# Optimization experiments

Measured on AMD Instinct MI355X. Metric: run time of the kernel, lower is better.

Reference implementation:

```python
import jax, jax.numpy as jnp
import numpy as np

EPS = 1e-10


def _gcn(X, A, W, act):
    # A_hat = A + I; symmetric normalization D^{-1/2} A_hat D^{-1/2}
    N = A.shape[0]
    A_hat = A + jnp.eye(N, dtype=A.dtype)
    d = 1.0 / jnp.sqrt(jnp.sum(A_hat, axis=1) + EPS)
    A_norm = (d[:, None] * A_hat) * d[None, :]  # same math as diag @ A_hat @ diag
    return act(A_norm @ (X @ W))


def _pool(X, A, s, k):
    scores = (X @ s)[:, 0]            # [N]
    _, idx = jax.lax.top_k(scores, k)  # static k (ceil(ratio*N))
    return X[idx], A[idx][:, idx], idx


def _unpool(Xp, idx, N):
    return jnp.zeros((N, Xp.shape[-1]), Xp.dtype).at[idx].set(Xp)


def _glorot(key, shape):
    lim = np.sqrt(6.0 / (shape[0] + shape[1])).astype(np.float32)
    return jax.random.uniform(key, shape, jnp.float32, -lim, lim)


def setup_inputs() -> dict:
    key = jax.random.key(0)
    ks = jax.random.split(key, 8)
    N, F_IN, F, C = 8192, 16, 32, 2
    x = jax.random.normal(ks[0], (N, F_IN), jnp.float32)
    # sparse-ish symmetric binary adjacency stored densely (as the module expects)
    a = (jax.random.uniform(ks[1], (N, N)) < 0.01).astype(jnp.float32)
    a = jnp.maximum(a, a.T)
    return {
        "x": x,
        "a": a,
        "W1": _glorot(ks[2], (F_IN, F)),
        "W2": _glorot(ks[3], (F, F)),
        "W3": _glorot(ks[4], (F, F)),
        "W4": _glorot(ks[5], (F, C)),
        "s1": _glorot(ks[6], (F, 1)),
        "s2": _glorot(ks[7], (F, 1)),
    }


def reference(x, a, W1, W2, W3, W4, s1, s2):
    N = x.shape[0]
    K1 = int(np.ceil(0.5 * N))   # pool1 ratio 0.5
    K2 = int(np.ceil(0.5 * K1))  # pool2 ratio 0.5
    relu = jax.nn.relu
    X1 = _gcn(x, a, W1, relu)                     # [N, F]
    X1p, A1p, idx1 = _pool(X1, a, s1, K1)         # [K1, F], [K1, K1]
    X2 = _gcn(X1p, A1p, W2, relu)                 # [K1, F]
    X2p, _, idx2 = _pool(X2, A1p, s2, K2)         # [K2, F]
    X3 = _unpool(X2p, idx2, K1)                   # scatter back to [K1, F]
    X3 = _gcn(X3, A1p, W3, relu)
    X4 = _unpool(X3, idx1, N)                     # scatter back to [N, F]
    return _gcn(X4, a, W4, lambda z: jax.nn.softmax(z, axis=-1))
```

## Files before the change

### kernel.cpp

```cpp
#include <hip/hip_runtime.h>
#include <stdint.h>

#define NNODES 8192
#define KP1 4096
#define KP2 2048
#define FIN 16
#define FH 32
#define COUT 2
#define STRA 320
#define STRS 320
#define CGRID 1024
#define GRPSH 5
#define GRPSZ 32
#define BARWORDS (66 * 32)
#define RNONE 0xFFFFu

typedef unsigned short u16;
typedef unsigned int u32;
typedef unsigned long long u64;

__device__ __forceinline__ void st_u32(void* p, u32 v)
{
    __hip_atomic_store((u32*)p, v, __ATOMIC_RELAXED, __HIP_MEMORY_SCOPE_AGENT);
}
__device__ __forceinline__ void st_f32(float* p, float v) { st_u32(p, __float_as_uint(v)); }
__device__ __forceinline__ void st_u64(void* p, u64 v)
{
    __hip_atomic_store((u64*)p, v, __ATOMIC_RELAXED, __HIP_MEMORY_SCOPE_AGENT);
}

__global__ __launch_bounds__(256) void build_ell(const float* __restrict__ A, int n, int stride,
        u16* __restrict__ ell, int* __restrict__ rowcnt, int* __restrict__ diag, float* __restrict__ dnorm,
        const float* __restrict__ Xf, const float* __restrict__ Wf, float* __restrict__ Zf, int kf,
        u32* __restrict__ bar)
{
    if ((int)blockIdx.x >= n) {
        if ((int)blockIdx.x == n) {
            for (int w = threadIdx.x; w < BARWORDS; w += 256)
                __hip_atomic_store(&bar[w], 0u, __ATOMIC_RELAXED, __HIP_MEMORY_SCOPE_AGENT);
        }
        int t = ((int)blockIdx.x - n) * 256 + threadIdx.x;
        int i = t >> 5;
        int f = t & 31;
        const float* xr = Xf + (size_t)i * kf;
        float acc = 0.0f;
        for (int k = 0; k < kf; ++k) acc += xr[k] * Wf[k * 32 + f];
        Zf[t] = acc;
        return;
    }
    __shared__ int cnt;
    __shared__ int dg;
    int row = blockIdx.x;
    if (threadIdx.x == 0) { cnt = 0; dg = 0; }
    __syncthreads();
    const float4* arow4 = (const float4*)(A + (size_t)row * n);
    u16* erow = ell + (size_t)row * stride;
    int n4 = n >> 2;
    for (int c4 = threadIdx.x; c4 < n4; c4 += 256) {
        float4 v = arow4[c4];
        if (v.x == 0.0f && v.y == 0.0f && v.z == 0.0f && v.w == 0.0f) continue;
        int cb = c4 << 2;
        if (v.x != 0.0f) {
            if (cb == row) dg = 1;
            else { int p = atomicAdd(&cnt, 1); if (p < stride) erow[p] = (u16)cb; }
        }
        if (v.y != 0.0f) {
            int c = cb + 1;
            if (c == row) dg = 1;
            else { int p = atomicAdd(&cnt, 1); if (p < stride) erow[p] = (u16)c; }
        }
        if (v.z != 0.0f) {
            int c = cb + 2;
            if (c == row) dg = 1;
            else { int p = atomicAdd(&cnt, 1); if (p < stride) erow[p] = (u16)c; }
        }
        if (v.w != 0.0f) {
            int c = cb + 3;
            if (c == row) dg = 1;
            else { int p = atomicAdd(&cnt, 1); if (p < stride) erow[p] = (u16)c; }
        }
    }
    __syncthreads();
    if (threadIdx.x == 0) {
        int cf = cnt;
        rowcnt[row] = cf < stride ? cf : stride;
        diag[row] = dg;
        dnorm[row] = rsqrtf((float)(cf + dg + 1) + 1e-10f);
    }
}

__device__ __forceinline__ void gbar(u32* bar, int bid, int nblk)
{
    __syncthreads();
    if (threadIdx.x == 0) {
        asm volatile("s_waitcnt vmcnt(0)" ::: "memory");
        int g = bid >> GRPSH;
        int ngrp = (nblk + GRPSZ - 1) >> GRPSH;
        int gsz = nblk - (g << GRPSH); if (gsz > GRPSZ) gsz = GRPSZ;
        u32* gcnt = bar + (size_t)g * 32;
        u32* ggen = bar + (size_t)(32 + g) * 32;
        u32* rcnt = bar + (size_t)64 * 32;
        u32* rgen = bar + (size_t)65 * 32;
        u32 sg = __hip_atomic_load(ggen, __ATOMIC_RELAXED, __HIP_MEMORY_SCOPE_AGENT);
        u32 a = __hip_atomic_fetch_add(gcnt, 1u, __ATOMIC_RELAXED, __HIP_MEMORY_SCOPE_AGENT);
        if (a == (u32)(gsz - 1)) {
            u32 sr = __hip_atomic_load(rgen, __ATOMIC_RELAXED, __HIP_MEMORY_SCOPE_AGENT);
            u32 r = __hip_atomic_fetch_add(rcnt, 1u, __ATOMIC_RELAXED, __HIP_MEMORY_SCOPE_AGENT);
            if (r == (u32)(ngrp - 1)) {
                __hip_atomic_store(rcnt, 0u, __ATOMIC_RELAXED, __HIP_MEMORY_SCOPE_AGENT);
                __hip_atomic_fetch_add(rgen, 1u, __ATOMIC_RELAXED, __HIP_MEMORY_SCOPE_AGENT);
            } else {
                while (__hip_atomic_load(rgen, __ATOMIC_RELAXED, __HIP_MEMORY_SCOPE_AGENT) == sr)
                    __builtin_amdgcn_s_sleep(2);
            }
            __hip_atomic_store(gcnt, 0u, __ATOMIC_RELAXED, __HIP_MEMORY_SCOPE_AGENT);
            __hip_atomic_fetch_add(ggen, 1u, __ATOMIC_RELAXED, __HIP_MEMORY_SCOPE_AGENT);
        } else {
            while (__hip_atomic_load(ggen, __ATOMIC_RELAXED, __HIP_MEMORY_SCOPE_AGENT) == sg)
                __builtin_amdgcn_s_sleep(4);
        }
    }
    __syncthreads();
}

struct TkS {
    u32 hist[4][256];
    u32 wsum[4];
    u32 pref;
    u32 rem;
};

__device__ __forceinline__ u32 km_of(float f)
{
    u32 u = __float_as_uint(f);
    u32 m;
    if (u & 0x80000000u) m = ~u; else m = u | 0x80000000u;
    return ~m;
}

__device__ void topk_local(TkS& s, u16* rank_l, u16* idx_l,
                           const float* __restrict__ scores, int n, int K, int tid,
                           int* __restrict__ grank, int* __restrict__ gidx, bool mirror)
{
    int wv = tid >> 6;
    int lane = tid & 63;
    int per = n >> 8;
    int base = tid * per;
    if (tid == 0) { s.pref = 0u; s.rem = (u32)K; }
    __syncthreads();
    for (int bp = 3; bp >= 0; --bp) {
        s.hist[0][tid] = 0u;
        s.hist[1][tid] = 0u;
        s.hist[2][tid] = 0u;
        s.hist[3][tid] = 0u;
        __syncthreads();
        u32 maskhi = 0u;
        if (bp < 3) maskhi = 0xFFFFFFFFu << ((bp + 1) * 8);
        u32 pref = s.pref;
        u32 rem = s.rem;
        for (int e = 0; e < per; ++e) {
            u32 km = km_of(scores[base + e]);
            if ((km & maskhi) == pref) atomicAdd(&s.hist[wv][(km >> (bp * 8)) & 255u], 1u);
        }
        __syncthreads();
        u32 tot = s.hist[0][tid] + s.hist[1][tid] + s.hist[2][tid] + s.hist[3][tid];
        u32 vv = tot;
        u32 t2;
        t2 = __shfl(vv, lane - 1);  if (lane >= 1)  vv += t2;
        t2 = __shfl(vv, lane - 2);  if (lane >= 2)  vv += t2;
        t2 = __shfl(vv, lane - 4);  if (lane >= 4)  vv += t2;
        t2 = __shfl(vv, lane - 8);  if (lane >= 8)  vv += t2;
        t2 = __shfl(vv, lane - 16); if (lane >= 16) vv += t2;
        t2 = __shfl(vv, lane - 32); if (lane >= 32) vv += t2;
        if (lane == 63) s.wsum[wv] = vv;
        __syncthreads();
        u32 add = 0u;
        if (wv > 0) add += s.wsum[0];
        if (wv > 1) add += s.wsum[1];
        if (wv > 2) add += s.wsum[2];
        u32 cum = vv + add;
        if (tot != 0u && cum >= rem && cum - tot < rem) {
            s.pref = pref | ((u32)tid << (bp * 8));
            s.rem = rem - (cum - tot);
        }
    }
    __syncthreads();
    u32 T = s.pref;
    u32 need_eq = s.rem;
    u32 run = 0u;
    for (int e = 0; e < per; ++e) {
        u32 km = km_of(scores[base + e]);
        if (km < T) run += 0x10000u;
        else if (km == T) run += 1u;
    }
    u32 v2 = run;
    u32 t3;
    t3 = __shfl(v2, lane - 1);  if (lane >= 1)  v2 += t3;
    t3 = __shfl(v2, lane - 2);  if (lane >= 2)  v2 += t3;
    t3 = __shfl(v2, lane - 4);  if (lane >= 4)  v2 += t3;
    t3 = __shfl(v2, lane - 8);  if (lane >= 8)  v2 += t3;
    t3 = __shfl(v2, lane - 16); if (lane >= 16) v2 += t3;
    t3 = __shfl(v2, lane - 32); if (lane >= 32) v2 += t3;
    if (lane == 63) s.wsum[wv] = v2;
    __syncthreads();
    u32 add2 = 0u;
    if (wv > 0) add2 += s.wsum[0];
    if (wv > 1) add2 += s.wsum[1];
    if (wv > 2) add2 += s.wsum[2];
    u32 cur = v2 + add2 - run;
    for (int e = 0; e < per; ++e) {
        int v = base + e;
        u32 km = km_of(scores[v]);
        u32 ltb = cur >> 16;
        u32 eqb = cur & 0xFFFFu;
        u32 eqs = eqb < need_eq ? eqb : need_eq;
        int sel = 0;
        if (km < T) { sel = 1; cur += 0x10000u; }
        else if (km == T) { if (eqb < need_eq) sel = 1; cur += 1u; }
        if (sel) {
            int r = (int)(ltb + eqs);
            rank_l[v] = (u16)r;
            idx_l[r] = (u16)v;
            if (mirror) { st_u32(&grank[v], (u32)r); st_u32(&gidx[r], (u32)v); }
        } else {
            rank_l[v] = RNONE;
            if (mirror) st_u32(&grank[v], 0xFFFFFFFFu);
        }
    }
    __syncthreads();
}

template<typename ET, bool REMAP, bool MASK, bool FW4, bool SC, bool EPI>
__device__ __forceinline__ void spmm_phase(
        const ET* __restrict__ ell, const int* __restrict__ rowcnt,
        const int* __restrict__ diag, const float* __restrict__ dnorm,
        const float* __restrict__ Z, const int* __restrict__ remap, const u16* mask_l,
        float* __restrict__ scores, const float* __restrict__ svec,
        const float* __restrict__ Wn, float* __restrict__ Zn,
        int n, int stride, int gwave, int nwaves, int lane)
{
    int g = lane >> 3;
    int q = lane & 7;
    for (int wid = gwave; wid < n; wid += nwaves) {
        int cnt = rowcnt[wid];
        const ET* erow = ell + (size_t)wid * stride;
        float ax = 0.0f, ay = 0.0f, az = 0.0f, aw = 0.0f;
        for (int it = g; it < cnt; it += 8) {
            int c = (int)erow[it];
            if (MASK && mask_l[c] == RNONE) continue;
            int zc = REMAP ? remap[c] : c;
            float dn = dnorm[c];
            const float4* zp = (const float4*)(Z + (size_t)zc * 32);
            float4 zv = zp[q];
            ax += dn * zv.x;
            ay += dn * zv.y;
            az += dn * zv.z;
            aw += dn * zv.w;
        }
        ax += __shfl_xor(ax, 8);  ay += __shfl_xor(ay, 8);
        az += __shfl_xor(az, 8);  aw += __shfl_xor(aw, 8);
        ax += __shfl_xor(ax, 16); ay += __shfl_xor(ay, 16);
        az += __shfl_xor(az, 16); aw += __shfl_xor(aw, 16);
        ax += __shfl_xor(ax, 32); ay += __shfl_xor(ay, 32);
        az += __shfl_xor(az, 32); aw += __shfl_xor(aw, 32);
        float ox = 0.0f, oy = 0.0f, oz = 0.0f, ow = 0.0f;
        if (g == 0) {
            float dr = dnorm[wid];
            bool selfok = !(MASK && mask_l[wid] == RNONE);
            if (selfok) {
                int zc = REMAP ? remap[wid] : wid;
                const float4* zp = (const float4*)(Z + (size_t)zc * 32);
                float4 zv = zp[q];
                float cf = (float)(diag[wid] + 1) * dr;
                ax += cf * zv.x;
                ay += cf * zv.y;
                az += cf * zv.z;
                aw += cf * zv.w;
            }
            ox = fmaxf(dr * ax, 0.0f);
            oy = fmaxf(dr * ay, 0.0f);
            oz = fmaxf(dr * az, 0.0f);
            ow = fmaxf(dr * aw, 0.0f);
            if (FW4) {
                int kb = q * 4;
                float p0 = ox * Wn[(kb + 0) * 2 + 0] + oy * Wn[(kb + 1) * 2 + 0]
                         + oz * Wn[(kb + 2) * 2 + 0] + ow * Wn[(kb + 3) * 2 + 0];
                float p1 = ox * Wn[(kb + 0) * 2 + 1] + oy * Wn[(kb + 1) * 2 + 1]
                         + oz * Wn[(kb + 2) * 2 + 1] + ow * Wn[(kb + 3) * 2 + 1];
                p0 += __shfl_xor(p0, 1);
                p1 += __shfl_xor(p1, 1);
                p0 += __shfl_xor(p0, 2);
                p1 += __shfl_xor(p1, 2);
                p0 += __shfl_xor(p0, 4);
                p1 += __shfl_xor(p1, 4);
                if (q == 0) {
                    union { float2 f; u64 u; } cv;
                    cv.f.x = p0;
                    cv.f.y = p1;
                    st_u64(&((float2*)Zn)[wid], cv.u);
                }
            } else if (SC) {
                const float4* sp = (const float4*)svec;
                float4 sv = sp[q];
                float pp = ox * sv.x + oy * sv.y + oz * sv.z + ow * sv.w;
                pp += __shfl_xor(pp, 1);
                pp += __shfl_xor(pp, 2);
                pp += __shfl_xor(pp, 4);
                if (q == 0) st_f32(&scores[wid], pp);
            }
        }
        if (EPI) {
            int f = lane & 31;
            float acc = 0.0f;
#pragma unroll
            for (int k = 0; k < 32; ++k) {
                float comp = ((k & 3) == 0) ? ox : ((k & 3) == 1) ? oy
                           : ((k & 3) == 2) ? oz : ow;
                float rowk = __shfl(comp, k >> 2);
                acc += rowk * Wn[k * 32 + f];
            }
            if (lane < 32) st_f32(&Zn[(size_t)wid * 32 + f], acc);
        }
    }
}

__device__ __forceinline__ void subell_phase(const u16* __restrict__ ellA, const int* __restrict__ rowcntA,
        const int* __restrict__ diagA, const u16* idx_l, const u16* rank_l,
        u32* __restrict__ ellS, int* __restrict__ rowcntS, int* __restrict__ diagS, float* __restrict__ dnormS,
        int k1, int strideA, int strideS, int gwave, int nwaves, int lane)
{
    for (int wid = gwave; wid < k1; wid += nwaves) {
        int r = idx_l[wid];
        int cnt = rowcntA[r];
        const u16* erow = ellA + (size_t)r * strideA;
        u32* srow = ellS + (size_t)wid * strideS;
        int outn = 0;
        for (int t0 = 0; t0 < cnt; t0 += 64) {
            int it = t0 + lane;
            u16 rk = RNONE;
            if (it < cnt) rk = rank_l[erow[it]];
            unsigned long long b = __ballot(rk != RNONE);
            int ofs = __popcll(b & ((1ull << lane) - 1ull));
            if (rk != RNONE) st_u32(&srow[outn + ofs], (u32)rk);
            outn += __popcll(b);
        }
        if (lane == 0) {
            int dg = diagA[r];
            st_u32(&rowcntS[wid], (u32)outn);
            st_u32(&diagS[wid], (u32)dg);
            st_f32(&dnormS[wid], rsqrtf((float)(outn + dg + 1) + 1e-10f));
        }
    }
}

__device__ __forceinline__ void spmmout_phase(const u16* __restrict__ ell, const int* __restrict__ rowcnt,
        const int* __restrict__ diag, const float* __restrict__ dnorm, const float* __restrict__ Zr,
        const int* __restrict__ gat, float* __restrict__ out, int n, int stride,
        int gwave, int nwaves, int lane)
{
    const float2* Z2 = (const float2*)Zr;
    for (int wid = gwave; wid < n; wid += nwaves) {
        int cnt = rowcnt[wid];
        const u16* erow = ell + (size_t)wid * stride;
        float ax = 0.0f, ay = 0.0f;
        for (int it = lane; it < cnt; it += 64) {
            int c = erow[it];
            int rk = gat[c];
            if (rk >= 0) {
                float dn = dnorm[c];
                float2 zv = Z2[rk];
                ax += dn * zv.x;
                ay += dn * zv.y;
            }
        }
        ax += __shfl_xor(ax, 1);  ay += __shfl_xor(ay, 1);
        ax += __shfl_xor(ax, 2);  ay += __shfl_xor(ay, 2);
        ax += __shfl_xor(ax, 4);  ay += __shfl_xor(ay, 4);
        ax += __shfl_xor(ax, 8);  ay += __shfl_xor(ay, 8);
        ax += __shfl_xor(ax, 16); ay += __shfl_xor(ay, 16);
        ax += __shfl_xor(ax, 32); ay += __shfl_xor(ay, 32);
        if (lane == 0) {
            float dr = dnorm[wid];
            int rks = gat[wid];
            if (rks >= 0) {
                float cf = (float)(diag[wid] + 1) * dr;
                float2 zs = Z2[rks];
                ax += cf * zs.x;
                ay += cf * zs.y;
            }
            float v0 = dr * ax;
            float v1 = dr * ay;
            float m = fmaxf(v0, v1);
            float e0 = __expf(v0 - m);
            float e1 = __expf(v1 - m);
            float inv = 1.0f / (e0 + e1);
            float2 r;
            r.x = e0 * inv;
            r.y = e1 * inv;
            ((float2*)out)[wid] = r;
        }
    }
}

struct GcnP {
    const u16* ellA; const int* cntA; const int* diagA; const float* dnA;
    const float* Z1; float* sc1; int* rank1; int* idx1;
    u32* ellS; int* cntS; int* diagS; float* dnS;
    float* Z2f; float* sc2;
    float* Z3f; float* Z4r;
    const float* W2; const float* W3; const float* W4; const float* s1; const float* s2;
    float* out;
    u32* bar;
};

__global__ __launch_bounds__(256, 4) void gcn_pipeline(GcnP p)
{
    __shared__ TkS sm;
    __shared__ u16 rank_l[NNODES];
    __shared__ u16 idx_l[KP1];
    int tid = threadIdx.x;
    int bid = blockIdx.x;
    int lane = tid & 63;
    int gwave = (bid * 256 + tid) >> 6;
    int nwaves = ((int)gridDim.x * 256) >> 6;
    int nblk = (int)gridDim.x;

    spmm_phase<u16, false, false, false, true, true>(p.ellA, p.cntA, p.diagA, p.dnA, p.Z1,
        (const int*)0, (const u16*)0, p.sc1, p.s1, p.W2, p.Z2f,
        NNODES, STRA, gwave, nwaves, lane);
    gbar(p.bar, bid, nblk);

    topk_local(sm, rank_l, idx_l, p.sc1, NNODES, KP1, tid, p.rank1, p.idx1, bid == 0);
    subell_phase(p.ellA, p.cntA, p.diagA, idx_l, rank_l, p.ellS, p.cntS, p.diagS, p.dnS,
        KP1, STRA, STRS, gwave, nwaves, lane);
    gbar(p.bar, bid, nblk);

    spmm_phase<u32, true, false, false, true, true>(p.ellS, p.cntS, p.diagS, p.dnS, p.Z2f,
        p.idx1, (const u16*)0, p.sc2, p.s2, p.W3, p.Z3f,
        KP1, STRS, gwave, nwaves, lane);
    gbar(p.bar, bid, nblk);

    topk_local(sm, rank_l, idx_l, p.sc2, KP1, KP2, tid, (int*)0, (int*)0, false);
    spmm_phase<u32, false, true, true, false, false>(p.ellS, p.cntS, p.diagS, p.dnS, p.Z3f,
        (const int*)0, rank_l, (float*)0, (const float*)0, p.W4, p.Z4r,
        KP1, STRS, gwave, nwaves, lane);
    gbar(p.bar, bid, nblk);

    spmmout_phase(p.ellA, p.cntA, p.diagA, p.dnA, p.Z4r, p.rank1, p.out,
        NNODES, STRA, gwave, nwaves, lane);
}

__global__ __launch_bounds__(256) void k_spmmA(const u16* __restrict__ ell, const int* __restrict__ rowcnt,
        const int* __restrict__ diag, const float* __restrict__ dnorm, const float* __restrict__ Z,
        float* __restrict__ scores, const float* __restrict__ svec,
        const float* __restrict__ Wn, float* __restrict__ Zn, int n, int stride)
{
    int gwave = ((int)blockIdx.x * 256 + (int)threadIdx.x) >> 6;
    int nwaves = ((int)gridDim.x * 256) >> 6;
    spmm_phase<u16, false, false, false, true, true>(ell, rowcnt, diag, dnorm, Z,
        (const int*)0, (const u16*)0, scores, svec, Wn, Zn, n, stride, gwave, nwaves, threadIdx.x & 63);
}

__global__ __launch_bounds__(256) void k_phaseB(const float* __restrict__ scores,
        int* __restrict__ grank, int* __restrict__ gidx,
        const u16* __restrict__ ellA, const int* __restrict__ rowcntA, const int* __restrict__ diagA,
        u32* __restrict__ ellS, int* __restrict__ rowcntS, int* __restrict__ diagS, float* __restrict__ dnormS)
{
    __shared__ TkS sm;
    __shared__ u16 rank_l[NNODES];
    __shared__ u16 idx_l[KP1];
    int gwave = ((int)blockIdx.x * 256 + (int)threadIdx.x) >> 6;
    int nwaves = ((int)gridDim.x * 256) >> 6;
    topk_local(sm, rank_l, idx_l, scores, NNODES, KP1, threadIdx.x, grank, gidx, blockIdx.x == 0);
    subell_phase(ellA, rowcntA, diagA, idx_l, rank_l, ellS, rowcntS, diagS, dnormS,
        KP1, STRA, STRS, gwave, nwaves, threadIdx.x & 63);
}

__global__ __launch_bounds__(256) void k_spmmC(const u32* __restrict__ ell, const int* __restrict__ rowcnt,
        const int* __restrict__ diag, const float* __restrict__ dnorm, const float* __restrict__ Z,
        const int* __restrict__ remap, float* __restrict__ scores, const float* __restrict__ svec,
        const float* __restrict__ Wn, float* __restrict__ Zn, int n, int stride)
{
    int gwave = ((int)blockIdx.x * 256 + (int)threadIdx.x) >> 6;
    int nwaves = ((int)gridDim.x * 256) >> 6;
    spmm_phase<u32, true, false, false, true, true>(ell, rowcnt, diag, dnorm, Z,
        remap, (const u16*)0, scores, svec, Wn, Zn, n, stride, gwave, nwaves, threadIdx.x & 63);
}

__global__ __launch_bounds__(256) void k_phaseD(const float* __restrict__ scores,
        const u32* __restrict__ ell, const int* __restrict__ rowcnt,
        const int* __restrict__ diag, const float* __restrict__ dnorm, const float* __restrict__ Z,
        const float* __restrict__ Wn, float* __restrict__ Zn, int n, int stride)
{
    __shared__ TkS sm;
    __shared__ u16 rank_l[NNODES];
    __shared__ u16 idx_l[KP1];
    int gwave = ((int)blockIdx.x * 256 + (int)threadIdx.x) >> 6;
    int nwaves = ((int)gridDim.x * 256) >> 6;
    topk_local(sm, rank_l, idx_l, scores, KP1, KP2, threadIdx.x, (int*)0, (int*)0, false);
    spmm_phase<u32, false, true, true, false, false>(ell, rowcnt, diag, dnorm, Z,
        (const int*)0, rank_l, (float*)0, (const float*)0, Wn, Zn, n, stride, gwave, nwaves, threadIdx.x & 63);
}

__global__ __launch_bounds__(256) void k_spmmout(const u16* __restrict__ ell, const int* __restrict__ rowcnt,
        const int* __restrict__ diag, const float* __restrict__ dnorm, const float* __restrict__ Zr,
        const int* __restrict__ gat, float* __restrict__ out, int n, int stride)
{
    int gwave = ((int)blockIdx.x * 256 + (int)threadIdx.x) >> 6;
    int nwaves = ((int)gridDim.x * 256) >> 6;
    spmmout_phase(ell, rowcnt, diag, dnorm, Zr, gat, out, n, stride, gwave, nwaves, threadIdx.x & 63);
}

#define CARVE(type, name, bytes) \
    type name = (type)wp; wp += (((size_t)(bytes)) + 255) & ~((size_t)255);

extern "C" void kernel_launch(void* const* d_in, const int* in_sizes, int n_in,
                              void* d_out, int out_size, void* d_ws, size_t ws_size,
                              hipStream_t stream)
{
    const float* x  = (const float*)d_in[0];
    const float* a  = (const float*)d_in[1];
    const float* W1 = (const float*)d_in[2];
    const float* W2 = (const float*)d_in[3];
    const float* W3 = (const float*)d_in[4];
    const float* W4 = (const float*)d_in[5];
    const float* s1 = (const float*)d_in[6];
    const float* s2 = (const float*)d_in[7];
    float* out = (float*)d_out;
    (void)in_sizes; (void)n_in; (void)out_size; (void)ws_size;

    char* wp = (char*)d_ws;
    CARVE(u16*,   ellA,  (size_t)NNODES * STRA * sizeof(u16));
    CARVE(int*,   cntA,  NNODES * sizeof(int));
    CARVE(int*,   diagA, NNODES * sizeof(int));
    CARVE(float*, dnA,   NNODES * sizeof(float));
    CARVE(float*, Z1,    (size_t)NNODES * FH * sizeof(float));
    CARVE(float*, sc1,   NNODES * sizeof(float));
    CARVE(int*,   rank1, NNODES * sizeof(int));
    CARVE(int*,   idx1,  NNODES * sizeof(int));
    CARVE(u32*,   ellS,  (size_t)KP1 * STRS * sizeof(u32));
    CARVE(int*,   cntS,  KP1 * sizeof(int));
    CARVE(int*,   diagS, KP1 * sizeof(int));
    CARVE(float*, dnS,   KP1 * sizeof(float));
    CARVE(float*, Z2f,   (size_t)NNODES * FH * sizeof(float));
    CARVE(float*, sc2,   KP1 * sizeof(float));
    CARVE(float*, Z3f,   (size_t)KP1 * FH * sizeof(float));
    CARVE(float*, Z4r,   (size_t)KP1 * COUT * sizeof(float));
    CARVE(u32*,   barws, BARWORDS * sizeof(u32));

    build_ell<<<NNODES + (NNODES * FH) / 256, 256, 0, stream>>>(
        a, NNODES, STRA, ellA, cntA, diagA, dnA, x, W1, Z1, FIN, barws);

    static int g_ok = -1;
    if (g_ok < 0) {
        int maxb = 0;
        int ncu = 0;
        hipDeviceProp_t props;
        if (hipOccupancyMaxActiveBlocksPerMultiprocessor(&maxb, (const void*)gcn_pipeline, 256, 0)
                == hipSuccess
            && hipGetDeviceProperties(&props, 0) == hipSuccess)
            ncu = props.multiProcessorCount;
        g_ok = ((long)maxb * (long)ncu >= CGRID) ? 1 : 0;
    }

    if (g_ok) {
        GcnP pp;
        pp.ellA = ellA; pp.cntA = cntA; pp.diagA = diagA; pp.dnA = dnA;
        pp.Z1 = Z1; pp.sc1 = sc1; pp.rank1 = rank1; pp.idx1 = idx1;
        pp.ellS = ellS; pp.cntS = cntS; pp.diagS = diagS; pp.dnS = dnS;
        pp.Z2f = Z2f; pp.sc2 = sc2;
        pp.Z3f = Z3f; pp.Z4r = Z4r;
        pp.W2 = W2; pp.W3 = W3; pp.W4 = W4; pp.s1 = s1; pp.s2 = s2;
        pp.out = out;
        pp.bar = barws;
        gcn_pipeline<<<CGRID, 256, 0, stream>>>(pp);
    } else {
        k_spmmA<<<NNODES / 4, 256, 0, stream>>>(ellA, cntA, diagA, dnA, Z1,
            sc1, s1, W2, Z2f, NNODES, STRA);
        k_phaseB<<<KP1 / 4, 256, 0, stream>>>(sc1, rank1, idx1,
            ellA, cntA, diagA, ellS, cntS, diagS, dnS);
        k_spmmC<<<KP1 / 4, 256, 0, stream>>>(ellS, cntS, diagS, dnS, Z2f,
            idx1, sc2, s2, W3, Z3f, KP1, STRS);
        k_phaseD<<<KP1 / 4, 256, 0, stream>>>(sc2, ellS, cntS, diagS, dnS, Z3f,
            W4, Z4r, KP1, STRS);
        k_spmmout<<<NNODES / 4, 256, 0, stream>>>(ellA, cntA, diagA, dnA, Z4r, rank1, out, NNODES, STRA);
    }
}
```

Measured before the change: 524.6 us.

## Fuse ELL construction into persistent pipeline and aggregate topk histogram atomics

Moves the dense-to-ELL adjacency conversion and the X@W1 product into the persistent cooperative kernel. Each block now processes 8 rows, staging column indices in shared memory and writing them out as packed u32 pairs, and a grid barrier separates this stage from the first SpMM. The barrier words are cleared with hipMemsetAsync instead of by the removed launch. Separately, the top-k radix histogram now uses wave-level ballot aggregation so each distinct bin gets one atomic per wave. The intent is to remove a kernel launch and reduce shared-atomic contention, but only 1024 blocks now stream the 256MB adjacency matrix instead of 8192, which may lower memory parallelism.

```diff
diff --git a/kernel.cpp b/kernel.cpp
--- a/kernel.cpp
+++ b/kernel.cpp
@@ -10,6 +10,7 @@
 #define STRA 320
 #define STRS 320
 #define CGRID 1024
+#define ROWS_PB (NNODES / CGRID)
 #define GRPSH 5
 #define GRPSZ 32
 #define BARWORDS (66 * 32)
@@ -27,66 +28,6 @@
 __device__ __forceinline__ void st_u64(void* p, u64 v)
 {
     __hip_atomic_store((u64*)p, v, __ATOMIC_RELAXED, __HIP_MEMORY_SCOPE_AGENT);
-}
-
-__global__ __launch_bounds__(256) void build_ell(const float* __restrict__ A, int n, int stride,
-        u16* __restrict__ ell, int* __restrict__ rowcnt, int* __restrict__ diag, float* __restrict__ dnorm,
-        const float* __restrict__ Xf, const float* __restrict__ Wf, float* __restrict__ Zf, int kf,
-        u32* __restrict__ bar)
-{
-    if ((int)blockIdx.x >= n) {
-        if ((int)blockIdx.x == n) {
-            for (int w = threadIdx.x; w < BARWORDS; w += 256)
-                __hip_atomic_store(&bar[w], 0u, __ATOMIC_RELAXED, __HIP_MEMORY_SCOPE_AGENT);
-        }
-        int t = ((int)blockIdx.x - n) * 256 + threadIdx.x;
-        int i = t >> 5;
-        int f = t & 31;
-        const float* xr = Xf + (size_t)i * kf;
-        float acc = 0.0f;
-        for (int k = 0; k < kf; ++k) acc += xr[k] * Wf[k * 32 + f];
-        Zf[t] = acc;
-        return;
-    }
-    __shared__ int cnt;
-    __shared__ int dg;
-    int row = blockIdx.x;
-    if (threadIdx.x == 0) { cnt = 0; dg = 0; }
-    __syncthreads();
-    const float4* arow4 = (const float4*)(A + (size_t)row * n);
-    u16* erow = ell + (size_t)row * stride;
-    int n4 = n >> 2;
-    for (int c4 = threadIdx.x; c4 < n4; c4 += 256) {
-        float4 v = arow4[c4];
-        if (v.x == 0.0f && v.y == 0.0f && v.z == 0.0f && v.w == 0.0f) continue;
-        int cb = c4 << 2;
-        if (v.x != 0.0f) {
-            if (cb == row) dg = 1;
-            else { int p = atomicAdd(&cnt, 1); if (p < stride) erow[p] = (u16)cb; }
-        }
-        if (v.y != 0.0f) {
-            int c = cb + 1;
-            if (c == row) dg = 1;
-            else { int p = atomicAdd(&cnt, 1); if (p < stride) erow[p] = (u16)c; }
-        }
-        if (v.z != 0.0f) {
-            int c = cb + 2;
-            if (c == row) dg = 1;
-            else { int p = atomicAdd(&cnt, 1); if (p < stride) erow[p] = (u16)c; }
-        }
-        if (v.w != 0.0f) {
-            int c = cb + 3;
-            if (c == row) dg = 1;
-            else { int p = atomicAdd(&cnt, 1); if (p < stride) erow[p] = (u16)c; }
-        }
-    }
-    __syncthreads();
-    if (threadIdx.x == 0) {
-        int cf = cnt;
-        rowcnt[row] = cf < stride ? cf : stride;
-        diag[row] = dg;
-        dnorm[row] = rsqrtf((float)(cf + dg + 1) + 1e-10f);
-    }
 }
 
 __device__ __forceinline__ void gbar(u32* bar, int bid, int nblk)
@@ -160,7 +101,16 @@
         u32 rem = s.rem;
         for (int e = 0; e < per; ++e) {
             u32 km = km_of(scores[base + e]);
-            if ((km & maskhi) == pref) atomicAdd(&s.hist[wv][(km >> (bp * 8)) & 255u], 1u);
+            bool prd = ((km & maskhi) == pref);
+            u32 bin = (km >> (bp * 8)) & 255u;
+            u64 todo = __ballot(prd);
+            while (todo) {
+                int ldr = __ffsll((long long)todo) - 1;
+                u32 lbin = __shfl(bin, ldr);
+                u64 same = __ballot(prd && (bin == lbin));
+                if (lane == ldr) atomicAdd(&s.hist[wv][lbin], (u32)__popcll(same));
+                todo &= ~same;
+            }
         }
         __syncthreads();
         u32 tot = s.hist[0][tid] + s.hist[1][tid] + s.hist[2][tid] + s.hist[3][tid];
@@ -403,8 +353,9 @@
 }
 
 struct GcnP {
-    const u16* ellA; const int* cntA; const int* diagA; const float* dnA;
-    const float* Z1; float* sc1; int* rank1; int* idx1;
+    const float* A; const float* x; const float* W1;
+    u16* ellA; int* cntA; int* diagA; float* dnA;
+    float* Z1; float* sc1; int* rank1; int* idx1;
     u32* ellS; int* cntS; int* diagS; float* dnS;
     float* Z2f; float* sc2;
     float* Z3f; float* Z4r;
@@ -418,6 +369,8 @@
     __shared__ TkS sm;
     __shared__ u16 rank_l[NNODES];
     __shared__ u16 idx_l[KP1];
+    __shared__ u16 colbuf[STRA];
+    __shared__ int scnt, sdg;
     int tid = threadIdx.x;
     int bid = blockIdx.x;
     int lane = tid & 63;
@@ -425,6 +378,65 @@
     int nwaves = ((int)gridDim.x * 256) >> 6;
     int nblk = (int)gridDim.x;
 
+    for (int rr = 0; rr < ROWS_PB; ++rr) {
+        int row = bid * ROWS_PB + rr;
+        if (tid == 0) { scnt = 0; sdg = 0; }
+        __syncthreads();
+        const float4* arow4 = (const float4*)(p.A + (size_t)row * NNODES);
+        int n4 = NNODES >> 2;
+        for (int c4 = tid; c4 < n4; c4 += 256) {
+            float4 v = arow4[c4];
+            if (v.x == 0.0f && v.y == 0.0f && v.z == 0.0f && v.w == 0.0f) continue;
+            int cb = c4 << 2;
+            if (v.x != 0.0f) {
+                if (cb == row) sdg = 1;
+                else { int pp = atomicAdd(&scnt, 1); if (pp < STRA) colbuf[pp] = (u16)cb; }
+            }
+            if (v.y != 0.0f) {
+                int c = cb + 1;
+                if (c == row) sdg = 1;
+                else { int pp = atomicAdd(&scnt, 1); if (pp < STRA) colbuf[pp] = (u16)c; }
+            }
+            if (v.z != 0.0f) {
+                int c = cb + 2;
+                if (c == row) sdg = 1;
+                else { int pp = atomicAdd(&scnt, 1); if (pp < STRA) colbuf[pp] = (u16)c; }
+            }
+            if (v.w != 0.0f) {
+                int c = cb + 3;
+                if (c == row) sdg = 1;
+                else { int pp = atomicAdd(&scnt, 1); if (pp < STRA) colbuf[pp] = (u16)c; }
+            }
+        }
+        __syncthreads();
+        int cf = scnt;
+        int dg = sdg;
+        int cw = cf < STRA ? cf : STRA;
+        u32* erow32 = (u32*)(p.ellA + (size_t)row * STRA);
+        int npair = (cw + 1) >> 1;
+        for (int t = tid; t < npair; t += 256) {
+            u32 lo = colbuf[2 * t];
+            u32 hi = (2 * t + 1 < cw) ? (u32)colbuf[2 * t + 1] : 0u;
+            st_u32(&erow32[t], lo | (hi << 16));
+        }
+        if (tid == 0) {
+            st_u32(&p.cntA[row], (u32)cw);
+            st_u32(&p.diagA[row], (u32)dg);
+            st_f32(&p.dnA[row], rsqrtf((float)(cf + dg + 1) + 1e-10f));
+        }
+        __syncthreads();
+    }
+    {
+        int t = bid * 256 + tid;
+        int i = t >> 5;
+        int f = t & 31;
+        const float* xr = p.x + (size_t)i * FIN;
+        float acc = 0.0f;
+        for (int k = 0; k < FIN; ++k) acc += xr[k] * p.W1[k * 32 + f];
+        st_f32(&p.Z1[t], acc);
+    }
+    gbar(p.bar, bid, nblk);
+
     spmm_phase<u16, false, false, false, true, true>(p.ellA, p.cntA, p.diagA, p.dnA, p.Z1,
         (const int*)0, (const u16*)0, p.sc1, p.s1, p.W2, p.Z2f,
         NNODES, STRA, gwave, nwaves, lane);
@@ -448,6 +460,61 @@
 
     spmmout_phase(p.ellA, p.cntA, p.diagA, p.dnA, p.Z4r, p.rank1, p.out,
         NNODES, STRA, gwave, nwaves, lane);
+}
+
+__global__ __launch_bounds__(256) void build_ell(const float* __restrict__ A, int n, int stride,
+        u16* __restrict__ ell, int* __restrict__ rowcnt, int* __restrict__ diag, float* __restrict__ dnorm,
+        const float* __restrict__ Xf, const float* __restrict__ Wf, float* __restrict__ Zf, int kf)
+{
+    if ((int)blockIdx.x >= n) {
+        int t = ((int)blockIdx.x - n) * 256 + threadIdx.x;
+        int i = t >> 5;
+        int f = t & 31;
+        const float* xr = Xf + (size_t)i * kf;
+        float acc = 0.0f;
+        for (int k = 0; k < kf; ++k) acc += xr[k] * Wf[k * 32 + f];
+        Zf[t] = acc;
+        return;
+    }
+    __shared__ int cnt;
+    __shared__ int dg;
+    int row = blockIdx.x;
+    if (threadIdx.x == 0) { cnt = 0; dg = 0; }
+    __syncthreads();
+    const float4* arow4 = (const float4*)(A + (size_t)row * n);
+    u16* erow = ell + (size_t)row * stride;
+    int n4 = n >> 2;
+    for (int c4 = threadIdx.x; c4 < n4; c4 += 256) {
+        float4 v = arow4[c4];
+        if (v.x == 0.0f && v.y == 0.0f && v.z == 0.0f && v.w == 0.0f) continue;
+        int cb = c4 << 2;
+        if (v.x != 0.0f) {
+            if (cb == row) dg = 1;
+            else { int pp = atomicAdd(&cnt, 1); if (pp < stride) erow[pp] = (u16)cb; }
+        }
+        if (v.y != 0.0f) {
+            int c = cb + 1;
+            if (c == row) dg = 1;
+            else { int pp = atomicAdd(&cnt, 1); if (pp < stride) erow[pp] = (u16)c; }
+        }
+        if (v.z != 0.0f) {
+            int c = cb + 2;
+            if (c == row) dg = 1;
+            else { int pp = atomicAdd(&cnt, 1); if (pp < stride) erow[pp] = (u16)c; }
+        }
+        if (v.w != 0.0f) {
+            int c = cb + 3;
+            if (c == row) dg = 1;
+            else { int pp = atomicAdd(&cnt, 1); if (pp < stride) erow[pp] = (u16)c; }
+        }
+    }
+    __syncthreads();
+    if (threadIdx.x == 0) {
+        int cf = cnt;
+        rowcnt[row] = cf < stride ? cf : stride;
+        diag[row] = dg;
+        dnorm[row] = rsqrtf((float)(cf + dg + 1) + 1e-10f);
+    }
 }
 
 __global__ __launch_bounds__(256) void k_spmmA(const u16* __restrict__ ell, const int* __restrict__ rowcnt,
@@ -548,8 +615,7 @@
     CARVE(float*, Z4r,   (size_t)KP1 * COUT * sizeof(float));
     CARVE(u32*,   barws, BARWORDS * sizeof(u32));
 
-    build_ell<<<NNODES + (NNODES * FH) / 256, 256, 0, stream>>>(
-        a, NNODES, STRA, ellA, cntA, diagA, dnA, x, W1, Z1, FIN, barws);
+    hipMemsetAsync(barws, 0, BARWORDS * sizeof(u32), stream);
 
     static int g_ok = -1;
     if (g_ok < 0) {
@@ -565,6 +631,7 @@
 
     if (g_ok) {
         GcnP pp;
+        pp.A = a; pp.x = x; pp.W1 = W1;
         pp.ellA = ellA; pp.cntA = cntA; pp.diagA = diagA; pp.dnA = dnA;
         pp.Z1 = Z1; pp.sc1 = sc1; pp.rank1 = rank1; pp.idx1 = idx1;
         pp.ellS = ellS; pp.cntS = cntS; pp.diagS = diagS; pp.dnS = dnS;
@@ -575,6 +642,8 @@
         pp.bar = barws;
         gcn_pipeline<<<CGRID, 256, 0, stream>>>(pp);
     } else {
+        build_ell<<<NNODES + (NNODES * FH) / 256, 256, 0, stream>>>(
+            a, NNODES, STRA, ellA, cntA, diagA, dnA, x, W1, Z1, FIN);
         k_spmmA<<<NNODES / 4, 256, 0, stream>>>(ellA, cntA, diagA, dnA, Z1,
             sc1, s1, W2, Z2f, NNODES, STRA);
         k_phaseB<<<KP1 / 4, 256, 0, stream>>>(sc1, rank1, idx1,
```

After: 701.7 us. 33.8% more time.
